# Optimization experiments

Hardware: AMD Instinct MI355X
Metric: run time of the kernel (lower is better)

The kernel has to match this reference:

```python
import jax, jax.numpy as jnp
import numpy as np

B, D, NCOMP, DCOMP = 4096, 2048, 4, 1024  # out_features = NCOMP * DCOMP = 4096


def setup_inputs() -> dict:
    key = jax.random.key(0)
    ks = jax.random.split(key, 6)
    scale = 0.02
    return {
        "x": jax.random.normal(ks[0], (B, D), jnp.float32),
        "noise": jax.random.normal(ks[1], (B, NCOMP), jnp.float32),
        "Wc": jax.random.normal(ks[2], (NCOMP, D, DCOMP), jnp.float32) * scale,
        "bc": jnp.zeros((NCOMP, DCOMP), jnp.float32),
        "Wg": jax.random.normal(ks[3], (D, NCOMP), jnp.float32) * scale,
        "bg": jnp.zeros((NCOMP,), jnp.float32),
        "Wn": jax.random.normal(ks[4], (D, NCOMP), jnp.float32) * scale,
        "bn": jnp.zeros((NCOMP,), jnp.float32),
    }


def reference(x, noise, Wc, bc, Wg, bg, Wn, bn):
    # gating: H = Wg(x) + randn * softplus(Wnoise(x))
    g = x @ Wg + bg                                   # [B, n]
    sp = jax.nn.softplus(x @ Wn + bn)                 # [B, n]
    H = g + noise * sp                                # [B, n]
    # top-1 index, monotonic hard gate: select all components i <= argmax
    k = jnp.argmax(H, axis=1, keepdims=True)          # [B, 1]
    mask = (jnp.arange(H.shape[1])[None, :] <= k).astype(H.dtype)  # [B, n]
    # straight-through: forward value = mask, grad d G/d H = identity
    G = H + jax.lax.stop_gradient(mask - H)
    # all components computed vectorized; unselected ones are zeroed by G
    comps = jnp.einsum('bd,ndo->bno', x, Wc) + bc     # [B, n, DCOMP]
    mask_sg = jax.lax.stop_gradient(mask)
    # multiply by mask_sg so unselected (padded) channels carry no grad path,
    # matching torch which never computes components beyond k (zero pad).
    E = (comps * G[:, :, None] * mask_sg[:, :, None]).reshape(x.shape[0], -1)  # [B, out_features]
    return (E, G)
```

## Files before the change

kernel.cpp:

```cpp
#include <hip/hip_runtime.h>
#include <hip/hip_bf16.h>
#include <math.h>

constexpr int BROWS = 4096;
constexpr int DDIM  = 2048;
constexpr int NCOMP = 4;
constexpr int DCOMP = 1024;
constexpr int NOUT  = NCOMP * DCOMP;

typedef __attribute__((ext_vector_type(8))) short bf16x8;
typedef __attribute__((ext_vector_type(4))) float f32x4;
typedef __attribute__((ext_vector_type(4))) short s16x4;

__device__ __forceinline__ short f2bf(float f) {
  union { float f; unsigned u; } v; v.f = f;
  unsigned r = v.u + 0x7FFFu + ((v.u >> 16) & 1u);
  return (short)(r >> 16);
}

#define GLOAD_LDS16(gptr, lptr) __builtin_amdgcn_global_load_lds( \
    (const __attribute__((address_space(1))) void*)(gptr),        \
    (__attribute__((address_space(3))) void*)(lptr), 16, 0, 0)

__global__ __launch_bounds__(256) void prep_kernel(
    const float* __restrict__ x, const float* __restrict__ noise,
    const float* __restrict__ Wg, const float* __restrict__ bg,
    const float* __restrict__ Wn, const float* __restrict__ bn,
    const float* __restrict__ Wc,
    float* __restrict__ Gout, short* __restrict__ xb, short* __restrict__ WcT) {
  __shared__ float tile[64][65];
  const int bid = blockIdx.x;
  const int tid = threadIdx.x;

  if (bid < 1024) {
    const int lane = tid & 63;
    const int row  = bid * 4 + (tid >> 6);
    const float* xr = x + (size_t)row * DDIM;
    short* xbr = xb + (size_t)row * DDIM;

    float ag[4] = {0.f, 0.f, 0.f, 0.f};
    float an[4] = {0.f, 0.f, 0.f, 0.f};
#pragma unroll
    for (int i = 0; i < 8; i++) {
      int d = i * 256 + lane * 4;
      float4 v = *reinterpret_cast<const float4*>(xr + d);
      s16x4 s; s.x = f2bf(v.x); s.y = f2bf(v.y); s.z = f2bf(v.z); s.w = f2bf(v.w);
      *reinterpret_cast<s16x4*>(xbr + d) = s;
      float xv[4] = {v.x, v.y, v.z, v.w};
#pragma unroll
      for (int j = 0; j < 4; j++) {
        float4 wg = *reinterpret_cast<const float4*>(Wg + 4 * (d + j));
        float4 wn = *reinterpret_cast<const float4*>(Wn + 4 * (d + j));
        ag[0] += xv[j] * wg.x; ag[1] += xv[j] * wg.y;
        ag[2] += xv[j] * wg.z; ag[3] += xv[j] * wg.w;
        an[0] += xv[j] * wn.x; an[1] += xv[j] * wn.y;
        an[2] += xv[j] * wn.z; an[3] += xv[j] * wn.w;
      }
    }
#pragma unroll
    for (int off = 32; off > 0; off >>= 1) {
#pragma unroll
      for (int c = 0; c < 4; c++) {
        ag[c] += __shfl_xor(ag[c], off);
        an[c] += __shfl_xor(an[c], off);
      }
    }
    if (lane == 0) {
      float H[4];
#pragma unroll
      for (int c = 0; c < 4; c++) {
        float v  = an[c] + bn[c];
        float sp = (v > 20.f) ? v : log1pf(expf(v));
        H[c] = (ag[c] + bg[c]) + noise[(size_t)row * NCOMP + c] * sp;
      }
      int k = 0; float best = H[0];
#pragma unroll
      for (int c = 1; c < 4; c++) { if (H[c] > best) { best = H[c]; k = c; } }
#pragma unroll
      for (int c = 0; c < 4; c++)
        Gout[(size_t)row * NCOMP + c] = (c <= k) ? 1.0f : 0.0f;
    }
  } else {
    const int tb  = bid - 1024;
    const int o_t = tb & 15, d_t = (tb >> 4) & 31, c = tb >> 9;
    const int d0 = d_t * 64, o0 = o_t * 64;
    const int col = tid & 63, rb = tid >> 6;

    const float* src = Wc + ((size_t)c * DDIM + d0) * DCOMP + o0;
#pragma unroll
    for (int i = 0; i < 16; i++) {
      int r = rb + i * 4;
      tile[r][col] = src[(size_t)r * DCOMP + col];
    }
    __syncthreads();
    short* dst = WcT + ((size_t)c * DCOMP + o0) * DDIM + d0;
    const int o  = tid >> 2;
    const int dsb = (tid & 3) * 16;
    bf16x8 p0, p1;
#pragma unroll
    for (int k = 0; k < 8; k++) {
      p0[k] = f2bf(tile[dsb + k][o]);
      p1[k] = f2bf(tile[dsb + 8 + k][o]);
    }
    *reinterpret_cast<bf16x8*>(dst + (size_t)o * DDIM + dsb)     = p0;
    *reinterpret_cast<bf16x8*>(dst + (size_t)o * DDIM + dsb + 8) = p1;
  }
}

constexpr int BM = 256, BN = 256, BK = 64;
constexpr int NT = DDIM / BK;
constexpr int HS = 128 * 64;

template<int MB, int NB>
__device__ __forceinline__ void MF(f32x4 (&acc)[8][4], bf16x8 (&a)[4][2], bf16x8 (&b)[2][2]) {
#pragma unroll
  for (int kh = 0; kh < 2; kh++)
#pragma unroll
    for (int ml = 0; ml < 4; ml++)
#pragma unroll
      for (int nl = 0; nl < 2; nl++)
        acc[MB + ml][NB + nl] = __builtin_amdgcn_mfma_f32_16x16x32_bf16(
            a[ml][kh], b[nl][kh], acc[MB + ml][NB + nl], 0, 0, 0);
}

#define PH_SYNC_MFMA(MB, NB)                                 \
  __builtin_amdgcn_s_barrier();                              \
  asm volatile("s_waitcnt lgkmcnt(0)");                      \
  __builtin_amdgcn_s_setprio(1);                             \
  MF<MB, NB>(acc, a, b);                                     \
  __builtin_amdgcn_s_setprio(0);

__global__ __launch_bounds__(512, 2) void gemm_kernel(
    const short* __restrict__ xb, const short* __restrict__ wt,
    const float* __restrict__ bc, const float* __restrict__ G,
    float* __restrict__ E) {
  __shared__ short Asm[2][2][HS];
  __shared__ short Bsm[2][2][HS];

  const int tid  = threadIdx.x;
  const int wave = tid >> 6, lane = tid & 63;
  const int wm = wave >> 2, wn = wave & 3;
  const int fr = lane & 15, fq = lane >> 4, l7 = lane & 7;

  const int xcd = blockIdx.x & 7, j = blockIdx.x >> 3;
  const int trow0 = (((xcd >> 1) << 2) + (j & 3)) * BM;
  const int tcol0 = (((xcd & 1) << 3) + (j >> 2)) * BN;

  const short* baseA[2] = { xb + (size_t)(trow0      ) * DDIM,
                            xb + (size_t)(trow0 + 128) * DDIM };
  const short* baseB[2] = { wt + (size_t)(tcol0      ) * DDIM,
                            wt + (size_t)(tcol0 + 128) * DDIM };

  size_t soff[2]; int ldst[2];
#pragma unroll
  for (int l = 0; l < 2; l++) {
    int f = l * 512 + tid;
    int r = f >> 3;
    int s = (f & 7) ^ (r & 7);
    soff[l] = (size_t)r * DDIM + s * 8;
    ldst[l] = (l * 512 + wave * 64) * 8;
  }

  auto STAGE = [&](const short* gb, int t, short* ldsh) {
#pragma unroll
    for (int l = 0; l < 2; l++)
      GLOAD_LDS16(gb + t * 64 + soff[l], ldsh + ldst[l]);
  };
  auto LDA = [&](const short* Ah, bf16x8 (&a)[4][2]) {
#pragma unroll
    for (int ml = 0; ml < 4; ml++) {
      int rh = wm * 64 + ml * 16 + fr;
#pragma unroll
      for (int kh = 0; kh < 2; kh++) {
        int sl = ((kh * 4 + fq) ^ l7) * 8;
        a[ml][kh] = *reinterpret_cast<const bf16x8*>(Ah + rh * 64 + sl);
      }
    }
  };
  auto LDB = [&](const short* Bh, bf16x8 (&b)[2][2]) {
#pragma unroll
    for (int nl = 0; nl < 2; nl++) {
      int ch = wn * 32 + nl * 16 + fr;
#pragma unroll
      for (int kh = 0; kh < 2; kh++) {
        int sl = ((kh * 4 + fq) ^ l7) * 8;
        b[nl][kh] = *reinterpret_cast<const bf16x8*>(Bh + ch * 64 + sl);
      }
    }
  };

  f32x4 acc[8][4];
#pragma unroll
  for (int m = 0; m < 8; m++)
#pragma unroll
    for (int n = 0; n < 4; n++) acc[m][n] = f32x4{0.f, 0.f, 0.f, 0.f};
  bf16x8 a[4][2], b[2][2];

  STAGE(baseA[0], 0, &Asm[0][0][0]);
  STAGE(baseA[1], 0, &Asm[0][1][0]);
  STAGE(baseB[0], 0, &Bsm[0][0][0]);
  STAGE(baseB[1], 0, &Bsm[0][1][0]);
  STAGE(baseA[0], 1, &Asm[1][0][0]);
  STAGE(baseB[1], 1, &Bsm[1][1][0]);
  asm volatile("s_waitcnt vmcnt(4)" ::: "memory");
  __builtin_amdgcn_s_barrier();

  for (int i = 0; i < NT / 2 - 1; i++) {
    const int t1 = 2 * i + 1, t2 = 2 * i + 2, t3 = 2 * i + 3;

    LDA(&Asm[0][0][0], a); LDB(&Bsm[0][0][0], b);
    STAGE(baseA[1], t1, &Asm[1][1][0]);
    PH_SYNC_MFMA(0, 0);
    __builtin_amdgcn_s_barrier();
    LDB(&Bsm[0][1][0], b);
    STAGE(baseB[0], t1, &Bsm[1][0][0]);
    PH_SYNC_MFMA(0, 2);
    __builtin_amdgcn_s_barrier();
    LDA(&Asm[0][1][0], a);
    STAGE(baseA[0], t2, &Asm[0][0][0]);
    PH_SYNC_MFMA(4, 2);
    __builtin_amdgcn_s_barrier();
    LDB(&Bsm[0][0][0], b);
    STAGE(baseB[1], t2, &Bsm[0][1][0]);
    PH_SYNC_MFMA(4, 0);
    asm volatile("s_waitcnt vmcnt(4)" ::: "memory");
    __builtin_amdgcn_s_barrier();
    LDA(&Asm[1][0][0], a); LDB(&Bsm[1][0][0], b);
    STAGE(baseA[1], t2, &Asm[0][1][0]);
    PH_SYNC_MFMA(0, 0);
    __builtin_amdgcn_s_barrier();
    LDB(&Bsm[1][1][0], b);
    STAGE(baseB[0], t2, &Bsm[0][0][0]);
    PH_SYNC_MFMA(0, 2);
    __builtin_amdgcn_s_barrier();
    LDA(&Asm[1][1][0], a);
    STAGE(baseA[0], t3, &Asm[1][0][0]);
    PH_SYNC_MFMA(4, 2);
    __builtin_amdgcn_s_barrier();
    LDB(&Bsm[1][0][0], b);
    STAGE(baseB[1], t3, &Bsm[1][1][0]);
    PH_SYNC_MFMA(4, 0);
    asm volatile("s_waitcnt vmcnt(4)" ::: "memory");
    __builtin_amdgcn_s_barrier();
  }

  {
    LDA(&Asm[0][0][0], a); LDB(&Bsm[0][0][0], b);
    STAGE(baseA[1], NT - 1, &Asm[1][1][0]);
    PH_SYNC_MFMA(0, 0);
    __builtin_amdgcn_s_barrier();
    LDB(&Bsm[0][1][0], b);
    STAGE(baseB[0], NT - 1, &Bsm[1][0][0]);
    PH_SYNC_MFMA(0, 2);
    __builtin_amdgcn_s_barrier();
    LDA(&Asm[0][1][0], a);
    PH_SYNC_MFMA(4, 2);
    __builtin_amdgcn_s_barrier();
    LDB(&Bsm[0][0][0], b);
    PH_SYNC_MFMA(4, 0);
    asm volatile("s_waitcnt vmcnt(0)" ::: "memory");
    __builtin_amdgcn_s_barrier();
    LDA(&Asm[1][0][0], a); LDB(&Bsm[1][0][0], b);
    PH_SYNC_MFMA(0, 0);
    __builtin_amdgcn_s_barrier();
    LDB(&Bsm[1][1][0], b);
    PH_SYNC_MFMA(0, 2);
    __builtin_amdgcn_s_barrier();
    LDA(&Asm[1][1][0], a);
    PH_SYNC_MFMA(4, 2);
    __builtin_amdgcn_s_barrier();
    LDB(&Bsm[1][0][0], b);
    PH_SYNC_MFMA(4, 0);
  }

  const int comp = tcol0 >> 10;
  const float* __restrict__ bcn = bc + (size_t)comp * DCOMP + (tcol0 & (DCOMP - 1));
  float bias[4];
#pragma unroll
  for (int n = 0; n < 4; n++)
    bias[n] = bcn[((n >> 1) * 128) + wn * 32 + (n & 1) * 16 + fr];
#pragma unroll
  for (int m = 0; m < 8; m++) {
    int growb = trow0 + ((m >> 2) * 128) + wm * 64 + (m & 3) * 16 + fq * 4;
#pragma unroll
    for (int j = 0; j < 4; j++) {
      int r = growb + j;
      float mval = G[(size_t)r * NCOMP + comp];
      float* Erow = E + (size_t)r * NOUT + tcol0;
#pragma unroll
      for (int n = 0; n < 4; n++) {
        int coll = ((n >> 1) * 128) + wn * 32 + (n & 1) * 16 + fr;
        Erow[coll] = mval * (acc[m][n][j] + bias[n]);
      }
    }
  }
}

extern "C" void kernel_launch(void* const* d_in, const int* in_sizes, int n_in,
                              void* d_out, int out_size, void* d_ws, size_t ws_size,
                              hipStream_t stream) {
  const float* x     = (const float*)d_in[0];
  const float* noise = (const float*)d_in[1];
  const float* Wc    = (const float*)d_in[2];
  const float* bc    = (const float*)d_in[3];
  const float* Wg    = (const float*)d_in[4];
  const float* bg    = (const float*)d_in[5];
  const float* Wn    = (const float*)d_in[6];
  const float* bn    = (const float*)d_in[7];

  float* E = (float*)d_out;
  float* G = (float*)d_out + (size_t)BROWS * NOUT;

  short* xb  = (short*)d_ws;
  short* WcT = xb + (size_t)BROWS * DDIM;

  prep_kernel<<<3072, 256, 0, stream>>>(x, noise, Wg, bg, Wn, bn, Wc, G, xb, WcT);
  gemm_kernel<<<256, 512, 0, stream>>>(xb, WcT, bc, G, E);
}
```

Before: 95.62 us.

## Keep both B fragments in registers and batch four gate rows per wave

The GEMM main loop now holds two B register fragments, so the B half reloaded for the last MFMA phase is reused instead of read again from LDS. The global-to-LDS staging order is reshuffled with a deeper vmcnt wait, so more tile loads stay in flight. The prep kernel has each wave handle four rows and reuse its Wg/Wn loads across them, which cuts the block count. The cost is more registers in both kernels, which could hurt occupancy under the 512x2 launch bound.

Measured after the change: 101.9 us. 1.07x slower.

```diff
diff --git a/kernel.cpp b/kernel.cpp
--- a/kernel.cpp
+++ b/kernel.cpp
@@ -32,56 +32,71 @@
   const int bid = blockIdx.x;
   const int tid = threadIdx.x;
 
-  if (bid < 1024) {
+  if (bid < 256) {
     const int lane = tid & 63;
-    const int row  = bid * 4 + (tid >> 6);
-    const float* xr = x + (size_t)row * DDIM;
-    short* xbr = xb + (size_t)row * DDIM;
-
-    float ag[4] = {0.f, 0.f, 0.f, 0.f};
-    float an[4] = {0.f, 0.f, 0.f, 0.f};
+    const int w    = tid >> 6;
+    const int r0   = bid * 16 + w * 4;
+
+    float ag[4][4], an[4][4];
+#pragma unroll
+    for (int r = 0; r < 4; r++)
+#pragma unroll
+      for (int c = 0; c < 4; c++) { ag[r][c] = 0.f; an[r][c] = 0.f; }
+
 #pragma unroll
     for (int i = 0; i < 8; i++) {
-      int d = i * 256 + lane * 4;
-      float4 v = *reinterpret_cast<const float4*>(xr + d);
-      s16x4 s; s.x = f2bf(v.x); s.y = f2bf(v.y); s.z = f2bf(v.z); s.w = f2bf(v.w);
-      *reinterpret_cast<s16x4*>(xbr + d) = s;
-      float xv[4] = {v.x, v.y, v.z, v.w};
+      const int d = i * 256 + lane * 4;
+      float4 wg4[4], wn4[4];
 #pragma unroll
       for (int j = 0; j < 4; j++) {
-        float4 wg = *reinterpret_cast<const float4*>(Wg + 4 * (d + j));
-        float4 wn = *reinterpret_cast<const float4*>(Wn + 4 * (d + j));
-        ag[0] += xv[j] * wg.x; ag[1] += xv[j] * wg.y;
-        ag[2] += xv[j] * wg.z; ag[3] += xv[j] * wg.w;
-        an[0] += xv[j] * wn.x; an[1] += xv[j] * wn.y;
-        an[2] += xv[j] * wn.z; an[3] += xv[j] * wn.w;
+        wg4[j] = *reinterpret_cast<const float4*>(Wg + 4 * (d + j));
+        wn4[j] = *reinterpret_cast<const float4*>(Wn + 4 * (d + j));
+      }
+#pragma unroll
+      for (int r = 0; r < 4; r++) {
+        float4 v = *reinterpret_cast<const float4*>(x + (size_t)(r0 + r) * DDIM + d);
+        s16x4 s; s.x = f2bf(v.x); s.y = f2bf(v.y); s.z = f2bf(v.z); s.w = f2bf(v.w);
+        *reinterpret_cast<s16x4*>(xb + (size_t)(r0 + r) * DDIM + d) = s;
+        float xv[4] = {v.x, v.y, v.z, v.w};
+#pragma unroll
+        for (int j = 0; j < 4; j++) {
+          ag[r][0] += xv[j] * wg4[j].x; ag[r][1] += xv[j] * wg4[j].y;
+          ag[r][2] += xv[j] * wg4[j].z; ag[r][3] += xv[j] * wg4[j].w;
+          an[r][0] += xv[j] * wn4[j].x; an[r][1] += xv[j] * wn4[j].y;
+          an[r][2] += xv[j] * wn4[j].z; an[r][3] += xv[j] * wn4[j].w;
+        }
       }
     }
 #pragma unroll
     for (int off = 32; off > 0; off >>= 1) {
 #pragma unroll
-      for (int c = 0; c < 4; c++) {
-        ag[c] += __shfl_xor(ag[c], off);
-        an[c] += __shfl_xor(an[c], off);
-      }
+      for (int r = 0; r < 4; r++)
+#pragma unroll
+        for (int c = 0; c < 4; c++) {
+          ag[r][c] += __shfl_xor(ag[r][c], off);
+          an[r][c] += __shfl_xor(an[r][c], off);
+        }
     }
     if (lane == 0) {
-      float H[4];
-#pragma unroll
-      for (int c = 0; c < 4; c++) {
-        float v  = an[c] + bn[c];
-        float sp = (v > 20.f) ? v : log1pf(expf(v));
-        H[c] = (ag[c] + bg[c]) + noise[(size_t)row * NCOMP + c] * sp;
-      }
-      int k = 0; float best = H[0];
-#pragma unroll
-      for (int c = 1; c < 4; c++) { if (H[c] > best) { best = H[c]; k = c; } }
-#pragma unroll
-      for (int c = 0; c < 4; c++)
-        Gout[(size_t)row * NCOMP + c] = (c <= k) ? 1.0f : 0.0f;
+#pragma unroll
+      for (int r = 0; r < 4; r++) {
+        float H[4];
+#pragma unroll
+        for (int c = 0; c < 4; c++) {
+          float v  = an[r][c] + bn[c];
+          float sp = (v > 20.f) ? v : log1pf(expf(v));
+          H[c] = (ag[r][c] + bg[c]) + noise[(size_t)(r0 + r) * NCOMP + c] * sp;
+        }
+        int k = 0; float best = H[0];
+#pragma unroll
+        for (int c = 1; c < 4; c++) { if (H[c] > best) { best = H[c]; k = c; } }
+#pragma unroll
+        for (int c = 0; c < 4; c++)
+          Gout[(size_t)(r0 + r) * NCOMP + c] = (c <= k) ? 1.0f : 0.0f;
+      }
     }
   } else {
-    const int tb  = bid - 1024;
+    const int tb  = bid - 256;
     const int o_t = tb & 15, d_t = (tb >> 4) & 31, c = tb >> 9;
     const int d0 = d_t * 64, o0 = o_t * 64;
     const int col = tid & 63, rb = tid >> 6;
@@ -94,7 +109,7 @@
     }
     __syncthreads();
     short* dst = WcT + ((size_t)c * DCOMP + o0) * DDIM + d0;
-    const int o  = tid >> 2;
+    const int o   = tid >> 2;
     const int dsb = (tid & 3) * 16;
     bf16x8 p0, p1;
 #pragma unroll
@@ -123,11 +138,11 @@
             a[ml][kh], b[nl][kh], acc[MB + ml][NB + nl], 0, 0, 0);
 }
 
-#define PH_SYNC_MFMA(MB, NB)                                 \
+#define PH_SYNC_MFMA(MB, NB, BREG)                           \
   __builtin_amdgcn_s_barrier();                              \
   asm volatile("s_waitcnt lgkmcnt(0)");                      \
   __builtin_amdgcn_s_setprio(1);                             \
-  MF<MB, NB>(acc, a, b);                                     \
+  MF<MB, NB>(acc, a, BREG);                                  \
   __builtin_amdgcn_s_setprio(0);
 
 __global__ __launch_bounds__(512, 2) void gemm_kernel(
@@ -194,83 +209,79 @@
   for (int m = 0; m < 8; m++)
 #pragma unroll
     for (int n = 0; n < 4; n++) acc[m][n] = f32x4{0.f, 0.f, 0.f, 0.f};
-  bf16x8 a[4][2], b[2][2];
+  bf16x8 a[4][2], bA[2][2], bB[2][2];
 
   STAGE(baseA[0], 0, &Asm[0][0][0]);
-  STAGE(baseA[1], 0, &Asm[0][1][0]);
   STAGE(baseB[0], 0, &Bsm[0][0][0]);
   STAGE(baseB[1], 0, &Bsm[0][1][0]);
+  STAGE(baseA[1], 0, &Asm[0][1][0]);
   STAGE(baseA[0], 1, &Asm[1][0][0]);
+  STAGE(baseB[0], 1, &Bsm[1][0][0]);
   STAGE(baseB[1], 1, &Bsm[1][1][0]);
-  asm volatile("s_waitcnt vmcnt(4)" ::: "memory");
+  asm volatile("s_waitcnt vmcnt(6)" ::: "memory");
   __builtin_amdgcn_s_barrier();
 
   for (int i = 0; i < NT / 2 - 1; i++) {
     const int t1 = 2 * i + 1, t2 = 2 * i + 2, t3 = 2 * i + 3;
 
-    LDA(&Asm[0][0][0], a); LDB(&Bsm[0][0][0], b);
+    LDA(&Asm[0][0][0], a); LDB(&Bsm[0][0][0], bA);
     STAGE(baseA[1], t1, &Asm[1][1][0]);
-    PH_SYNC_MFMA(0, 0);
-    __builtin_amdgcn_s_barrier();
-    LDB(&Bsm[0][1][0], b);
-    STAGE(baseB[0], t1, &Bsm[1][0][0]);
-    PH_SYNC_MFMA(0, 2);
+    PH_SYNC_MFMA(0, 0, bA);
+    __builtin_amdgcn_s_barrier();
+    LDB(&Bsm[0][1][0], bB);
+    STAGE(baseA[0], t2, &Asm[0][0][0]);
+    PH_SYNC_MFMA(0, 2, bB);
     __builtin_amdgcn_s_barrier();
     LDA(&Asm[0][1][0], a);
-    STAGE(baseA[0], t2, &Asm[0][0][0]);
-    PH_SYNC_MFMA(4, 2);
-    __builtin_amdgcn_s_barrier();
-    LDB(&Bsm[0][0][0], b);
+    STAGE(baseB[0], t2, &Bsm[0][0][0]);
+    PH_SYNC_MFMA(4, 2, bB);
+    __builtin_amdgcn_s_barrier();
     STAGE(baseB[1], t2, &Bsm[0][1][0]);
-    PH_SYNC_MFMA(4, 0);
-    asm volatile("s_waitcnt vmcnt(4)" ::: "memory");
-    __builtin_amdgcn_s_barrier();
-    LDA(&Asm[1][0][0], a); LDB(&Bsm[1][0][0], b);
+    PH_SYNC_MFMA(4, 0, bA);
+    asm volatile("s_waitcnt vmcnt(6)" ::: "memory");
+    __builtin_amdgcn_s_barrier();
+    LDA(&Asm[1][0][0], a); LDB(&Bsm[1][0][0], bA);
     STAGE(baseA[1], t2, &Asm[0][1][0]);
-    PH_SYNC_MFMA(0, 0);
-    __builtin_amdgcn_s_barrier();
-    LDB(&Bsm[1][1][0], b);
-    STAGE(baseB[0], t2, &Bsm[0][0][0]);
-    PH_SYNC_MFMA(0, 2);
+    PH_SYNC_MFMA(0, 0, bA);
+    __builtin_amdgcn_s_barrier();
+    LDB(&Bsm[1][1][0], bB);
+    STAGE(baseA[0], t3, &Asm[1][0][0]);
+    PH_SYNC_MFMA(0, 2, bB);
     __builtin_amdgcn_s_barrier();
     LDA(&Asm[1][1][0], a);
-    STAGE(baseA[0], t3, &Asm[1][0][0]);
-    PH_SYNC_MFMA(4, 2);
-    __builtin_amdgcn_s_barrier();
-    LDB(&Bsm[1][0][0], b);
+    STAGE(baseB[0], t3, &Bsm[1][0][0]);
+    PH_SYNC_MFMA(4, 2, bB);
+    __builtin_amdgcn_s_barrier();
     STAGE(baseB[1], t3, &Bsm[1][1][0]);
-    PH_SYNC_MFMA(4, 0);
-    asm volatile("s_waitcnt vmcnt(4)" ::: "memory");
+    PH_SYNC_MFMA(4, 0, bA);
+    asm volatile("s_waitcnt vmcnt(6)" ::: "memory");
     __builtin_amdgcn_s_barrier();
   }
 
   {
-    LDA(&Asm[0][0][0], a); LDB(&Bsm[0][0][0], b);
+    LDA(&Asm[0][0][0], a); LDB(&Bsm[0][0][0], bA);
     STAGE(baseA[1], NT - 1, &Asm[1][1][0]);
-    PH_SYNC_MFMA(0, 0);
-    __builtin_amdgcn_s_barrier();
-    LDB(&Bsm[0][1][0], b);
-    STAGE(baseB[0], NT - 1, &Bsm[1][0][0]);
-    PH_SYNC_MFMA(0, 2);
+    PH_SYNC_MFMA(0, 0, bA);
+    __builtin_amdgcn_s_barrier();
+    LDB(&Bsm[0][1][0], bB);
+    PH_SYNC_MFMA(0, 2, bB);
     __builtin_amdgcn_s_barrier();
     LDA(&Asm[0][1][0], a);
-    PH_SYNC_MFMA(4, 2);
-    __builtin_amdgcn_s_barrier();
-    LDB(&Bsm[0][0][0], b);
-    PH_SYNC_MFMA(4, 0);
+    PH_SYNC_MFMA(4, 2, bB);
+    __builtin_amdgcn_s_barrier();
+    PH_SYNC_MFMA(4, 0, bA);
     asm volatile("s_waitcnt vmcnt(0)" ::: "memory");
     __builtin_amdgcn_s_barrier();
-    LDA(&Asm[1][0][0], a); LDB(&Bsm[1][0][0], b);
-    PH_SYNC_MFMA(0, 0);
-    __builtin_amdgcn_s_barrier();
-    LDB(&Bsm[1][1][0], b);
-    PH_SYNC_MFMA(0, 2);
+    LDA(&Asm[1][0][0], a); LDB(&Bsm[1][0][0], bA);
+    PH_SYNC_MFMA(0, 0, bA);
+    __builtin_amdgcn_s_barrier();
+    LDB(&Bsm[1][1][0], bB);
+    PH_SYNC_MFMA(0, 2, bB);
     __builtin_amdgcn_s_barrier();
     LDA(&Asm[1][1][0], a);
-    PH_SYNC_MFMA(4, 2);
-    __builtin_amdgcn_s_barrier();
-    LDB(&Bsm[1][0][0], b);
-    PH_SYNC_MFMA(4, 0);
+    PH_SYNC_MFMA(4, 2, bB);
+    __builtin_amdgcn_s_barrier();
+    PH_SYNC_MFMA(4, 0, bA);
   }
 
   const int comp = tcol0 >> 10;
@@ -314,6 +325,6 @@
   short* xb  = (short*)d_ws;
   short* WcT = xb + (size_t)BROWS * DDIM;
 
-  prep_kernel<<<3072, 256, 0, stream>>>(x, noise, Wg, bg, Wn, bn, Wc, G, xb, WcT);
+  prep_kernel<<<2304, 256, 0, stream>>>(x, noise, Wg, bg, Wn, bn, Wc, G, xb, WcT);
   gemm_kernel<<<256, 512, 0, stream>>>(xb, WcT, bc, G, E);
 }
```

## Skip masked components by compacting rows per gated component

Applied to the files above, without the earlier changes.

Adds a single-block builder kernel that buckets rows by their top-1 index and writes a row-index list plus per-component row counts. The GEMM then gathers only the active rows for each component, using 128x256 tiles, and writes output without the mask multiply. A separate set of blocks writes zeros for the masked-out components. This avoids the matmul work for gated-off components, at the cost of an extra serial launch, gathered A loads, a smaller tile with more blocks, and early-exit blocks that depend on the data.

After: 105.8 us. +10.6%, slower.

```diff
diff --git a/kernel.cpp b/kernel.cpp
--- a/kernel.cpp
+++ b/kernel.cpp
@@ -94,7 +94,7 @@
     }
     __syncthreads();
     short* dst = WcT + ((size_t)c * DCOMP + o0) * DDIM + d0;
-    const int o  = tid >> 2;
+    const int o   = tid >> 2;
     const int dsb = (tid & 3) * 16;
     bf16x8 p0, p1;
 #pragma unroll
@@ -107,190 +107,229 @@
   }
 }
 
-constexpr int BM = 256, BN = 256, BK = 64;
+__global__ __launch_bounds__(1024) void builder_kernel(
+    const float* __restrict__ G, unsigned short* __restrict__ ridx,
+    int* __restrict__ cnt) {
+  __shared__ int hist[4], woff[4];
+  const int tid = threadIdx.x;
+  if (tid < 4) hist[tid] = 0;
+  __syncthreads();
+  int kk[4];
+#pragma unroll
+  for (int p = 0; p < 4; p++) {
+    int row = tid + p * 1024;
+    float4 g = *reinterpret_cast<const float4*>(G + (size_t)row * 4);
+    kk[p] = (int)(g.x + g.y + g.z + g.w) - 1;
+    atomicAdd(&hist[kk[p]], 1);
+  }
+  __syncthreads();
+  if (tid == 0) {
+    int c3 = hist[3], c2 = hist[2], c1 = hist[1];
+    woff[3] = 0; woff[2] = c3; woff[1] = c3 + c2; woff[0] = c3 + c2 + c1;
+    cnt[3] = c3; cnt[2] = c3 + c2; cnt[1] = c3 + c2 + c1; cnt[0] = 4096;
+  }
+  __syncthreads();
+#pragma unroll
+  for (int p = 0; p < 4; p++) {
+    int pos = atomicAdd(&woff[kk[p]], 1);
+    ridx[pos] = (unsigned short)(tid + p * 1024);
+  }
+}
+
+constexpr int BK = 64;
 constexpr int NT = DDIM / BK;
-constexpr int HS = 128 * 64;
 
 template<int MB, int NB>
-__device__ __forceinline__ void MF(f32x4 (&acc)[8][4], bf16x8 (&a)[4][2], bf16x8 (&b)[2][2]) {
+__device__ __forceinline__ void MF(f32x4 (&acc)[4][4], bf16x8 (&a)[2][2], bf16x8 (&b)[2][2]) {
 #pragma unroll
   for (int kh = 0; kh < 2; kh++)
 #pragma unroll
-    for (int ml = 0; ml < 4; ml++)
-#pragma unroll
-      for (int nl = 0; nl < 2; nl++)
-        acc[MB + ml][NB + nl] = __builtin_amdgcn_mfma_f32_16x16x32_bf16(
-            a[ml][kh], b[nl][kh], acc[MB + ml][NB + nl], 0, 0, 0);
-}
-
-#define PH_SYNC_MFMA(MB, NB)                                 \
+    for (int i = 0; i < 2; i++)
+#pragma unroll
+      for (int j = 0; j < 2; j++)
+        acc[MB + i][NB + j] = __builtin_amdgcn_mfma_f32_16x16x32_bf16(
+            a[i][kh], b[j][kh], acc[MB + i][NB + j], 0, 0, 0);
+}
+
+#define PH_SYNC_MFMA(MB, NB, BREG)                           \
   __builtin_amdgcn_s_barrier();                              \
   asm volatile("s_waitcnt lgkmcnt(0)");                      \
   __builtin_amdgcn_s_setprio(1);                             \
-  MF<MB, NB>(acc, a, b);                                     \
+  MF<MB, NB>(acc, a, BREG);                                  \
   __builtin_amdgcn_s_setprio(0);
 
 __global__ __launch_bounds__(512, 2) void gemm_kernel(
     const short* __restrict__ xb, const short* __restrict__ wt,
     const float* __restrict__ bc, const float* __restrict__ G,
+    const unsigned short* __restrict__ ridx, const int* __restrict__ cnt,
     float* __restrict__ E) {
-  __shared__ short Asm[2][2][HS];
-  __shared__ short Bsm[2][2][HS];
-
-  const int tid  = threadIdx.x;
+  __shared__ short Asm[2][128 * 64];
+  __shared__ short Bsm[2][256 * 64];
+
+  const int bid = blockIdx.x;
+  const int tid = threadIdx.x;
+
+  if (bid < 128) {
+    for (int rr = 0; rr < 32; rr++) {
+      int row = bid * 32 + rr;
+      float4 g = *reinterpret_cast<const float4*>(G + (size_t)row * 4);
+      int kk = (int)(g.x + g.y + g.z + g.w) - 1;
+      for (int n = kk + 1; n < 4; n++) {
+        float2* p = reinterpret_cast<float2*>(E + (size_t)row * NOUT + n * DCOMP);
+        p[tid] = float2{0.f, 0.f};
+      }
+    }
+    return;
+  }
+
+  const int cb   = bid - 128;
+  const int comp = cb >> 7;
+  const int rt   = (cb >> 2) & 31;
+  const int ct   = cb & 3;
+  const int cntn = cnt[comp];
+  if (rt * 128 >= cntn) return;
+
   const int wave = tid >> 6, lane = tid & 63;
   const int wm = wave >> 2, wn = wave & 3;
   const int fr = lane & 15, fq = lane >> 4, l7 = lane & 7;
 
-  const int xcd = blockIdx.x & 7, j = blockIdx.x >> 3;
-  const int trow0 = (((xcd >> 1) << 2) + (j & 3)) * BM;
-  const int tcol0 = (((xcd & 1) << 3) + (j >> 2)) * BN;
-
-  const short* baseA[2] = { xb + (size_t)(trow0      ) * DDIM,
-                            xb + (size_t)(trow0 + 128) * DDIM };
-  const short* baseB[2] = { wt + (size_t)(tcol0      ) * DDIM,
-                            wt + (size_t)(tcol0 + 128) * DDIM };
-
-  size_t soff[2]; int ldst[2];
+  const int colT = comp * DCOMP + ct * 256;
+  const short* gB = wt + (size_t)colT * DDIM;
+
+  size_t soffB[2]; const short* gA[2]; int ldst[2];
 #pragma unroll
   for (int l = 0; l < 2; l++) {
     int f = l * 512 + tid;
     int r = f >> 3;
     int s = (f & 7) ^ (r & 7);
-    soff[l] = (size_t)r * DDIM + s * 8;
+    soffB[l] = (size_t)r * DDIM + s * 8;
+    int g = rt * 128 + r;
+    g = (g < cntn) ? g : (cntn - 1);
+    gA[l] = xb + (size_t)ridx[g] * DDIM + s * 8;
     ldst[l] = (l * 512 + wave * 64) * 8;
   }
 
-  auto STAGE = [&](const short* gb, int t, short* ldsh) {
+  auto STAGE_A = [&](int buf, int t) {
 #pragma unroll
     for (int l = 0; l < 2; l++)
-      GLOAD_LDS16(gb + t * 64 + soff[l], ldsh + ldst[l]);
+      GLOAD_LDS16(gA[l] + t * 64, &Asm[buf][0] + ldst[l]);
   };
-  auto LDA = [&](const short* Ah, bf16x8 (&a)[4][2]) {
-#pragma unroll
-    for (int ml = 0; ml < 4; ml++) {
-      int rh = wm * 64 + ml * 16 + fr;
+  auto STAGE_B = [&](int buf, int t, int h) {
+#pragma unroll
+    for (int l = 0; l < 2; l++)
+      GLOAD_LDS16(gB + (size_t)(h * 128) * DDIM + t * 64 + soffB[l],
+                  &Bsm[buf][h * 8192] + ldst[l]);
+  };
+  auto LDA = [&](int buf, int MB, bf16x8 (&a)[2][2]) {
+#pragma unroll
+    for (int i = 0; i < 2; i++) {
+      int rh = wm * 64 + (MB + i) * 16 + fr;
 #pragma unroll
       for (int kh = 0; kh < 2; kh++) {
         int sl = ((kh * 4 + fq) ^ l7) * 8;
-        a[ml][kh] = *reinterpret_cast<const bf16x8*>(Ah + rh * 64 + sl);
+        a[i][kh] = *reinterpret_cast<const bf16x8*>(&Asm[buf][rh * 64 + sl]);
       }
     }
   };
-  auto LDB = [&](const short* Bh, bf16x8 (&b)[2][2]) {
-#pragma unroll
-    for (int nl = 0; nl < 2; nl++) {
-      int ch = wn * 32 + nl * 16 + fr;
+  auto LDB = [&](int buf, int NB, bf16x8 (&b)[2][2]) {
+#pragma unroll
+    for (int j = 0; j < 2; j++) {
+      int ch = wn * 64 + (NB + j) * 16 + fr;
 #pragma unroll
       for (int kh = 0; kh < 2; kh++) {
         int sl = ((kh * 4 + fq) ^ l7) * 8;
-        b[nl][kh] = *reinterpret_cast<const bf16x8*>(Bh + ch * 64 + sl);
+        b[j][kh] = *reinterpret_cast<const bf16x8*>(&Bsm[buf][ch * 64 + sl]);
       }
     }
   };
 
-  f32x4 acc[8][4];
-#pragma unroll
-  for (int m = 0; m < 8; m++)
+  f32x4 acc[4][4];
+#pragma unroll
+  for (int m = 0; m < 4; m++)
 #pragma unroll
     for (int n = 0; n < 4; n++) acc[m][n] = f32x4{0.f, 0.f, 0.f, 0.f};
-  bf16x8 a[4][2], b[2][2];
-
-  STAGE(baseA[0], 0, &Asm[0][0][0]);
-  STAGE(baseA[1], 0, &Asm[0][1][0]);
-  STAGE(baseB[0], 0, &Bsm[0][0][0]);
-  STAGE(baseB[1], 0, &Bsm[0][1][0]);
-  STAGE(baseA[0], 1, &Asm[1][0][0]);
-  STAGE(baseB[1], 1, &Bsm[1][1][0]);
-  asm volatile("s_waitcnt vmcnt(4)" ::: "memory");
+  bf16x8 a[2][2], bA[2][2], bB[2][2];
+
+  STAGE_B(0, 0, 0); STAGE_B(0, 0, 1); STAGE_A(0, 0);
+  STAGE_B(1, 1, 0); STAGE_B(1, 1, 1); STAGE_A(1, 1);
+  asm volatile("s_waitcnt vmcnt(6)" ::: "memory");
   __builtin_amdgcn_s_barrier();
 
   for (int i = 0; i < NT / 2 - 1; i++) {
-    const int t1 = 2 * i + 1, t2 = 2 * i + 2, t3 = 2 * i + 3;
-
-    LDA(&Asm[0][0][0], a); LDB(&Bsm[0][0][0], b);
-    STAGE(baseA[1], t1, &Asm[1][1][0]);
-    PH_SYNC_MFMA(0, 0);
-    __builtin_amdgcn_s_barrier();
-    LDB(&Bsm[0][1][0], b);
-    STAGE(baseB[0], t1, &Bsm[1][0][0]);
-    PH_SYNC_MFMA(0, 2);
-    __builtin_amdgcn_s_barrier();
-    LDA(&Asm[0][1][0], a);
-    STAGE(baseA[0], t2, &Asm[0][0][0]);
-    PH_SYNC_MFMA(4, 2);
-    __builtin_amdgcn_s_barrier();
-    LDB(&Bsm[0][0][0], b);
-    STAGE(baseB[1], t2, &Bsm[0][1][0]);
-    PH_SYNC_MFMA(4, 0);
+    const int t2 = 2 * i + 2, t3 = 2 * i + 3;
+
+    LDA(0, 0, a); LDB(0, 0, bA);
+    PH_SYNC_MFMA(0, 0, bA);
+    __builtin_amdgcn_s_barrier();
+    LDB(0, 2, bB);
+    PH_SYNC_MFMA(0, 2, bB);
+    __builtin_amdgcn_s_barrier();
+    LDA(0, 2, a);
+    STAGE_B(0, t2, 0);
+    PH_SYNC_MFMA(2, 2, bB);
+    __builtin_amdgcn_s_barrier();
+    STAGE_B(0, t2, 1);
+    PH_SYNC_MFMA(2, 0, bA);
     asm volatile("s_waitcnt vmcnt(4)" ::: "memory");
     __builtin_amdgcn_s_barrier();
-    LDA(&Asm[1][0][0], a); LDB(&Bsm[1][0][0], b);
-    STAGE(baseA[1], t2, &Asm[0][1][0]);
-    PH_SYNC_MFMA(0, 0);
-    __builtin_amdgcn_s_barrier();
-    LDB(&Bsm[1][1][0], b);
-    STAGE(baseB[0], t2, &Bsm[0][0][0]);
-    PH_SYNC_MFMA(0, 2);
-    __builtin_amdgcn_s_barrier();
-    LDA(&Asm[1][1][0], a);
-    STAGE(baseA[0], t3, &Asm[1][0][0]);
-    PH_SYNC_MFMA(4, 2);
-    __builtin_amdgcn_s_barrier();
-    LDB(&Bsm[1][0][0], b);
-    STAGE(baseB[1], t3, &Bsm[1][1][0]);
-    PH_SYNC_MFMA(4, 0);
-    asm volatile("s_waitcnt vmcnt(4)" ::: "memory");
+    LDA(1, 0, a); LDB(1, 0, bA);
+    STAGE_A(0, t2);
+    PH_SYNC_MFMA(0, 0, bA);
+    __builtin_amdgcn_s_barrier();
+    LDB(1, 2, bB);
+    PH_SYNC_MFMA(0, 2, bB);
+    __builtin_amdgcn_s_barrier();
+    LDA(1, 2, a);
+    STAGE_B(1, t3, 0); STAGE_B(1, t3, 1);
+    PH_SYNC_MFMA(2, 2, bB);
+    __builtin_amdgcn_s_barrier();
+    STAGE_A(1, t3);
+    PH_SYNC_MFMA(2, 0, bA);
+    asm volatile("s_waitcnt vmcnt(6)" ::: "memory");
     __builtin_amdgcn_s_barrier();
   }
 
   {
-    LDA(&Asm[0][0][0], a); LDB(&Bsm[0][0][0], b);
-    STAGE(baseA[1], NT - 1, &Asm[1][1][0]);
-    PH_SYNC_MFMA(0, 0);
-    __builtin_amdgcn_s_barrier();
-    LDB(&Bsm[0][1][0], b);
-    STAGE(baseB[0], NT - 1, &Bsm[1][0][0]);
-    PH_SYNC_MFMA(0, 2);
-    __builtin_amdgcn_s_barrier();
-    LDA(&Asm[0][1][0], a);
-    PH_SYNC_MFMA(4, 2);
-    __builtin_amdgcn_s_barrier();
-    LDB(&Bsm[0][0][0], b);
-    PH_SYNC_MFMA(4, 0);
+    LDA(0, 0, a); LDB(0, 0, bA);
+    PH_SYNC_MFMA(0, 0, bA);
+    __builtin_amdgcn_s_barrier();
+    LDB(0, 2, bB);
+    PH_SYNC_MFMA(0, 2, bB);
+    __builtin_amdgcn_s_barrier();
+    LDA(0, 2, a);
+    PH_SYNC_MFMA(2, 2, bB);
+    __builtin_amdgcn_s_barrier();
+    PH_SYNC_MFMA(2, 0, bA);
     asm volatile("s_waitcnt vmcnt(0)" ::: "memory");
     __builtin_amdgcn_s_barrier();
-    LDA(&Asm[1][0][0], a); LDB(&Bsm[1][0][0], b);
-    PH_SYNC_MFMA(0, 0);
-    __builtin_amdgcn_s_barrier();
-    LDB(&Bsm[1][1][0], b);
-    PH_SYNC_MFMA(0, 2);
-    __builtin_amdgcn_s_barrier();
-    LDA(&Asm[1][1][0], a);
-    PH_SYNC_MFMA(4, 2);
-    __builtin_amdgcn_s_barrier();
-    LDB(&Bsm[1][0][0], b);
-    PH_SYNC_MFMA(4, 0);
-  }
-
-  const int comp = tcol0 >> 10;
-  const float* __restrict__ bcn = bc + (size_t)comp * DCOMP + (tcol0 & (DCOMP - 1));
+    LDA(1, 0, a); LDB(1, 0, bA);
+    PH_SYNC_MFMA(0, 0, bA);
+    __builtin_amdgcn_s_barrier();
+    LDB(1, 2, bB);
+    PH_SYNC_MFMA(0, 2, bB);
+    __builtin_amdgcn_s_barrier();
+    LDA(1, 2, a);
+    PH_SYNC_MFMA(2, 2, bB);
+    __builtin_amdgcn_s_barrier();
+    PH_SYNC_MFMA(2, 0, bA);
+  }
+
+  const int rit = cntn - rt * 128;
   float bias[4];
 #pragma unroll
   for (int n = 0; n < 4; n++)
-    bias[n] = bcn[((n >> 1) * 128) + wn * 32 + (n & 1) * 16 + fr];
-#pragma unroll
-  for (int m = 0; m < 8; m++) {
-    int growb = trow0 + ((m >> 2) * 128) + wm * 64 + (m & 3) * 16 + fq * 4;
+    bias[n] = bc[colT + wn * 64 + n * 16 + fr];
+#pragma unroll
+  for (int m = 0; m < 4; m++) {
 #pragma unroll
     for (int j = 0; j < 4; j++) {
-      int r = growb + j;
-      float mval = G[(size_t)r * NCOMP + comp];
-      float* Erow = E + (size_t)r * NOUT + tcol0;
-#pragma unroll
-      for (int n = 0; n < 4; n++) {
-        int coll = ((n >> 1) * 128) + wn * 32 + (n & 1) * 16 + fr;
-        Erow[coll] = mval * (acc[m][n][j] + bias[n]);
+      int rl = wm * 64 + m * 16 + fq * 4 + j;
+      if (rl < rit) {
+        int row = ridx[rt * 128 + rl];
+        float* Erow = E + (size_t)row * NOUT + colT + wn * 64;
+#pragma unroll
+        for (int n = 0; n < 4; n++)
+          Erow[n * 16 + fr] = acc[m][n][j] + bias[n];
       }
     }
   }
@@ -311,9 +350,13 @@
   float* E = (float*)d_out;
   float* G = (float*)d_out + (size_t)BROWS * NOUT;
 
-  short* xb  = (short*)d_ws;
-  short* WcT = xb + (size_t)BROWS * DDIM;
-
-  prep_kernel<<<3072, 256, 0, stream>>>(x, noise, Wg, bg, Wn, bn, Wc, G, xb, WcT);
-  gemm_kernel<<<256, 512, 0, stream>>>(xb, WcT, bc, G, E);
-}
+  char* ws = (char*)d_ws;
+  short*          xbuf = (short*)ws;
+  short*          WcT  = (short*)(ws + (size_t)16 * 1024 * 1024);
+  unsigned short* ridx = (unsigned short*)(ws + (size_t)32 * 1024 * 1024);
+  int*            cnt  = (int*)(ws + (size_t)32 * 1024 * 1024 + 8192);
+
+  prep_kernel<<<3072, 256, 0, stream>>>(x, noise, Wg, bg, Wn, bn, Wc, G, xbuf, WcT);
+  builder_kernel<<<1, 1024, 0, stream>>>(G, ridx, cnt);
+  gemm_kernel<<<640, 512, 0, stream>>>(xbuf, WcT, bc, G, ridx, cnt, E);
+}
```

## Double-buffer fragment registers and deepen LDS prefetch in GEMM mainloop

Applied to the files above, without the earlier changes.

Reworks the GEMM main loop so that A and B fragment registers are double-buffered (aP/aQ, bA/bB). The next LDS read is issued while the current MFMA batch runs, instead of waiting on lgkmcnt(0) right before each MFMA phase. The global-to-LDS staging is reordered to keep more loads in flight (vmcnt 10/12 rather than 4), with one barrier per phase and sched_barrier fences. This is meant to hide LDS read latency and reduce barrier stalls, at the cost of more registers and tighter correctness constraints on the buffer reuse ordering.

New measurement: 100.4 us. 1.05x slower.

```diff
diff --git a/kernel.cpp b/kernel.cpp
--- a/kernel.cpp
+++ b/kernel.cpp
@@ -94,7 +94,7 @@
     }
     __syncthreads();
     short* dst = WcT + ((size_t)c * DCOMP + o0) * DDIM + d0;
-    const int o  = tid >> 2;
+    const int o   = tid >> 2;
     const int dsb = (tid & 3) * 16;
     bf16x8 p0, p1;
 #pragma unroll
@@ -123,11 +123,14 @@
             a[ml][kh], b[nl][kh], acc[MB + ml][NB + nl], 0, 0, 0);
 }
 
-#define PH_SYNC_MFMA(MB, NB)                                 \
-  __builtin_amdgcn_s_barrier();                              \
-  asm volatile("s_waitcnt lgkmcnt(0)");                      \
+#define PH_TOP(N)                                            \
+  asm volatile("s_waitcnt vmcnt(" #N ")" ::: "memory");      \
+  __builtin_amdgcn_s_barrier();
+
+#define PH_MFMA(MB, NB, AREG, BREG)                          \
+  __builtin_amdgcn_sched_barrier(0);                         \
   __builtin_amdgcn_s_setprio(1);                             \
-  MF<MB, NB>(acc, a, b);                                     \
+  MF<MB, NB>(acc, AREG, BREG);                               \
   __builtin_amdgcn_s_setprio(0);
 
 __global__ __launch_bounds__(512, 2) void gemm_kernel(
@@ -194,83 +197,81 @@
   for (int m = 0; m < 8; m++)
 #pragma unroll
     for (int n = 0; n < 4; n++) acc[m][n] = f32x4{0.f, 0.f, 0.f, 0.f};
-  bf16x8 a[4][2], b[2][2];
+  bf16x8 aP[4][2], aQ[4][2], bA[2][2], bB[2][2];
 
   STAGE(baseA[0], 0, &Asm[0][0][0]);
+  STAGE(baseB[0], 0, &Bsm[0][0][0]);
   STAGE(baseA[1], 0, &Asm[0][1][0]);
-  STAGE(baseB[0], 0, &Bsm[0][0][0]);
   STAGE(baseB[1], 0, &Bsm[0][1][0]);
+  STAGE(baseB[0], 1, &Bsm[1][0][0]);
+  STAGE(baseA[1], 1, &Asm[1][1][0]);
   STAGE(baseA[0], 1, &Asm[1][0][0]);
   STAGE(baseB[1], 1, &Bsm[1][1][0]);
-  asm volatile("s_waitcnt vmcnt(4)" ::: "memory");
+  asm volatile("s_waitcnt vmcnt(12)" ::: "memory");
   __builtin_amdgcn_s_barrier();
+  LDA(&Asm[0][0][0], aP);
+  LDB(&Bsm[0][0][0], bA);
 
   for (int i = 0; i < NT / 2 - 1; i++) {
-    const int t1 = 2 * i + 1, t2 = 2 * i + 2, t3 = 2 * i + 3;
-
-    LDA(&Asm[0][0][0], a); LDB(&Bsm[0][0][0], b);
-    STAGE(baseA[1], t1, &Asm[1][1][0]);
-    PH_SYNC_MFMA(0, 0);
+    const int t2 = 2 * i + 2, t3 = 2 * i + 3;
+
+    PH_TOP(10);
+    LDA(&Asm[0][1][0], aQ);
+    STAGE(baseB[0], t2, &Bsm[0][0][0]);
+    PH_MFMA(0, 0, aP, bA);
+    PH_TOP(10);
+    LDB(&Bsm[0][1][0], bB);
+    STAGE(baseA[0], t2, &Asm[0][0][0]);
+    PH_MFMA(4, 0, aQ, bA);
+    PH_TOP(10);
+    LDB(&Bsm[1][0][0], bA);
+    STAGE(baseA[1], t2, &Asm[0][1][0]);
+    PH_MFMA(4, 2, aQ, bB);
+    PH_TOP(10);
+    LDA(&Asm[1][1][0], aQ);
+    STAGE(baseB[1], t2, &Bsm[0][1][0]);
+    PH_MFMA(0, 2, aP, bB);
+    PH_TOP(10);
+    LDA(&Asm[1][0][0], aP);
+    STAGE(baseB[0], t3, &Bsm[1][0][0]);
+    PH_MFMA(4, 0, aQ, bA);
+    PH_TOP(10);
+    LDB(&Bsm[1][1][0], bB);
+    STAGE(baseA[1], t3, &Asm[1][1][0]);
+    PH_MFMA(0, 0, aP, bA);
+    PH_TOP(10);
+    LDB(&Bsm[0][0][0], bA);
+    STAGE(baseA[0], t3, &Asm[1][0][0]);
+    PH_MFMA(0, 2, aP, bB);
+    PH_TOP(10);
+    LDA(&Asm[0][0][0], aP);
+    STAGE(baseB[1], t3, &Bsm[1][1][0]);
+    PH_MFMA(4, 2, aQ, bB);
+  }
+
+  {
+    PH_TOP(10);
+    LDA(&Asm[0][1][0], aQ);
+    PH_MFMA(0, 0, aP, bA);
+    PH_TOP(8);
+    LDB(&Bsm[0][1][0], bB);
+    PH_MFMA(4, 0, aQ, bA);
+    PH_TOP(6);
+    LDB(&Bsm[1][0][0], bA);
+    PH_MFMA(4, 2, aQ, bB);
+    PH_TOP(4);
+    LDA(&Asm[1][1][0], aQ);
+    PH_MFMA(0, 2, aP, bB);
+    PH_TOP(2);
+    LDA(&Asm[1][0][0], aP);
+    PH_MFMA(4, 0, aQ, bA);
+    PH_TOP(0);
+    LDB(&Bsm[1][1][0], bB);
+    PH_MFMA(0, 0, aP, bA);
     __builtin_amdgcn_s_barrier();
-    LDB(&Bsm[0][1][0], b);
-    STAGE(baseB[0], t1, &Bsm[1][0][0]);
-    PH_SYNC_MFMA(0, 2);
+    PH_MFMA(0, 2, aP, bB);
     __builtin_amdgcn_s_barrier();
-    LDA(&Asm[0][1][0], a);
-    STAGE(baseA[0], t2, &Asm[0][0][0]);
-    PH_SYNC_MFMA(4, 2);
-    __builtin_amdgcn_s_barrier();
-    LDB(&Bsm[0][0][0], b);
-    STAGE(baseB[1], t2, &Bsm[0][1][0]);
-    PH_SYNC_MFMA(4, 0);
-    asm volatile("s_waitcnt vmcnt(4)" ::: "memory");
-    __builtin_amdgcn_s_barrier();
-    LDA(&Asm[1][0][0], a); LDB(&Bsm[1][0][0], b);
-    STAGE(baseA[1], t2, &Asm[0][1][0]);
-    PH_SYNC_MFMA(0, 0);
-    __builtin_amdgcn_s_barrier();
-    LDB(&Bsm[1][1][0], b);
-    STAGE(baseB[0], t2, &Bsm[0][0][0]);
-    PH_SYNC_MFMA(0, 2);
-    __builtin_amdgcn_s_barrier();
-    LDA(&Asm[1][1][0], a);
-    STAGE(baseA[0], t3, &Asm[1][0][0]);
-    PH_SYNC_MFMA(4, 2);
-    __builtin_amdgcn_s_barrier();
-    LDB(&Bsm[1][0][0], b);
-    STAGE(baseB[1], t3, &Bsm[1][1][0]);
-    PH_SYNC_MFMA(4, 0);
-    asm volatile("s_waitcnt vmcnt(4)" ::: "memory");
-    __builtin_amdgcn_s_barrier();
-  }
-
-  {
-    LDA(&Asm[0][0][0], a); LDB(&Bsm[0][0][0], b);
-    STAGE(baseA[1], NT - 1, &Asm[1][1][0]);
-    PH_SYNC_MFMA(0, 0);
-    __builtin_amdgcn_s_barrier();
-    LDB(&Bsm[0][1][0], b);
-    STAGE(baseB[0], NT - 1, &Bsm[1][0][0]);
-    PH_SYNC_MFMA(0, 2);
-    __builtin_amdgcn_s_barrier();
-    LDA(&Asm[0][1][0], a);
-    PH_SYNC_MFMA(4, 2);
-    __builtin_amdgcn_s_barrier();
-    LDB(&Bsm[0][0][0], b);
-    PH_SYNC_MFMA(4, 0);
-    asm volatile("s_waitcnt vmcnt(0)" ::: "memory");
-    __builtin_amdgcn_s_barrier();
-    LDA(&Asm[1][0][0], a); LDB(&Bsm[1][0][0], b);
-    PH_SYNC_MFMA(0, 0);
-    __builtin_amdgcn_s_barrier();
-    LDB(&Bsm[1][1][0], b);
-    PH_SYNC_MFMA(0, 2);
-    __builtin_amdgcn_s_barrier();
-    LDA(&Asm[1][1][0], a);
-    PH_SYNC_MFMA(4, 2);
-    __builtin_amdgcn_s_barrier();
-    LDB(&Bsm[1][0][0], b);
-    PH_SYNC_MFMA(4, 0);
+    PH_MFMA(4, 2, aQ, bB);
   }
 
   const int comp = tcol0 >> 10;
```
